# Performance work log

Measured on AMD Instinct MI355X. Metric: run time of the kernel, lower is better.

The kernel has to match this reference:

```python
import math
import jax, jax.numpy as jnp
from jax import lax
import numpy as np

NEG_INF = -1e9
LOG_2PI = math.log(2.0 * math.pi)


def compute_logp(z_p, m_p, logs_p):
    # z_p: [B,C,Ty], m_p/logs_p: [B,C,Tx] -> logp: [B,Tx,Ty]
    o_scale = jnp.exp(-2.0 * logs_p)                                  # [B,C,Tx]
    logp1 = jnp.sum(-0.5 * LOG_2PI - logs_p, axis=1)[:, :, None]      # [B,Tx,1]
    logp2 = jnp.einsum('bct,bcs->bts', o_scale, -0.5 * z_p ** 2)      # [B,Tx,Ty]
    logp3 = jnp.einsum('bct,bcs->bts', m_p * o_scale, z_p)            # [B,Tx,Ty]
    logp4 = jnp.sum(-0.5 * m_p ** 2 * o_scale, axis=1)[:, :, None]    # [B,Tx,1]
    return logp1 + logp2 + logp3 + logp4


def maximum_path(logp, mask):
    # Monotonic alignment search (Glow-TTS/VITS Viterbi DP).
    # logp, mask: [B,Tx,Ty]. Returns hard alignment path [B,Tx,Ty] in {0,1}.
    B, Tx, Ty = logp.shape
    tx = mask[:, :, 0].sum(axis=1).astype(jnp.int32)   # text lengths [B]
    ty = mask[:, 0, :].sum(axis=1).astype(jnp.int32)   # mel lengths  [B]
    xs = jnp.arange(Tx, dtype=jnp.int32)

    # ---- forward DP over mel frames y ----
    def fwd(v, inp):
        y, col = inp                                   # col: logp[:, :, y]  [B,Tx]
        v_stay = jnp.where(xs[None, :] == y, NEG_INF, v)           # can't stay on diagonal
        first = jnp.where(y == 0, 0.0, NEG_INF)                     # x==0 boundary
        v_move = jnp.concatenate([jnp.broadcast_to(first, (B, 1)).astype(v.dtype), v[:, :-1]], axis=1)
        newv = jnp.maximum(v_stay, v_move) + col
        # feasible band: x <= y and enough frames remain to consume all text
        feas = (xs[None, :] <= y) & (xs[None, :] >= tx[:, None] + y - ty[:, None])
        newv = jnp.where(feas, newv, NEG_INF)
        return newv, newv

    cols = jnp.moveaxis(logp, 2, 0)                    # [Ty,B,Tx]
    init = jnp.full((B, Tx), NEG_INF, dtype=logp.dtype)
    _, vals = lax.scan(fwd, init, (jnp.arange(Ty, dtype=jnp.int32), cols))  # [Ty,B,Tx]
    prev = jnp.concatenate([jnp.zeros((1, B, Tx), dtype=vals.dtype), vals[:-1]], axis=0)

    # ---- backtrack from (tx-1, ty-1) down to y=0 ----
    def bwd(idx, inp):
        y, pv = inp                                    # pv: value column at y-1  [B,Tx]
        active = y < ty                                # [B] bool
        path_col = (active[:, None] & (xs[None, :] == idx[:, None])).astype(logp.dtype)
        v_stay = jnp.take_along_axis(pv, idx[:, None], axis=1)[:, 0]
        v_move = jnp.take_along_axis(pv, jnp.maximum(idx - 1, 0)[:, None], axis=1)[:, 0]
        dec = (idx != 0) & ((idx == y) | (v_stay < v_move))
        idx = jnp.where(active & dec, idx - 1, idx)
        return idx, path_col

    _, path = lax.scan(bwd, tx - 1, (jnp.arange(Ty, dtype=jnp.int32), prev), reverse=True)
    return jnp.transpose(path, (1, 2, 0))              # [B,Tx,Ty]


def setup_inputs() -> dict:
    key = jax.random.key(0)
    ks = jax.random.split(key, 5)
    B, C, Tx, Ty = 16, 192, 384, 1536
    z_p = jax.random.normal(ks[0], (B, C, Ty), dtype=jnp.float32)
    m_p = jax.random.normal(ks[1], (B, C, Tx), dtype=jnp.float32)
    logs_p = 0.5 * jax.random.normal(ks[2], (B, C, Tx), dtype=jnp.float32)
    x_len = jax.random.randint(ks[3], (B,), Tx // 2, Tx + 1)
    y_len = jax.random.randint(ks[4], (B,), Ty // 2, Ty + 1)  # Ty//2 > Tx -> path always feasible
    x_mask = (jnp.arange(Tx)[None, :] < x_len[:, None]).astype(jnp.float32)[:, None, :]
    y_mask = (jnp.arange(Ty)[None, :] < y_len[:, None]).astype(jnp.float32)[:, None, :]
    return {"z_p": z_p, "m_p": m_p, "logs_p": logs_p, "x_mask": x_mask, "y_mask": y_mask}


def reference(z_p, m_p, logs_p, x_mask, y_mask):
    # forward_mas_without_dp: log-likelihood einsum + monotonic alignment search
    attn_mask = x_mask[:, 0, :, None] * y_mask[:, 0, None, :]   # [B,Tx,Ty]
    logp = compute_logp(z_p, m_p, logs_p)
    attn = maximum_path(logp, attn_mask)
    return attn[:, None]                                         # [B,1,Tx,Ty]
```

## Files before the change

### kernel.cpp

```cpp
#include <hip/hip_runtime.h>
#include <hip/hip_bf16.h>
#include <math.h>

#define NEG_INF (-1e9f)
#define B_   16
#define C_   192
#define TX   384
#define TY   1536
#define NWP  49
#define ROW_BYTES 1536

#define BM 64
#define BN 64
#define BK 16

typedef float f32x2 __attribute__((ext_vector_type(2)));
typedef float f32x4 __attribute__((ext_vector_type(4)));

__global__ __launch_bounds__(64) void k_len(const float* __restrict__ xm,
                                            const float* __restrict__ ym,
                                            int* __restrict__ lens) {
    const int b = blockIdx.x, l = threadIdx.x;
    int tx = 0, ty = 0;
#pragma unroll
    for (int i = 0; i < TX / 64; ++i)
        tx += __popcll(__ballot(xm[b * TX + i * 64 + l] > 0.5f));
#pragma unroll
    for (int i = 0; i < TY / 64; ++i)
        ty += __popcll(__ballot(ym[b * TY + i * 64 + l] > 0.5f));
    if (l == 0) { lens[2 * b] = tx; lens[2 * b + 1] = ty; }
}

__global__ __launch_bounds__(128) void k_rowconst(const float* __restrict__ m_p,
                                                  const float* __restrict__ logs_p,
                                                  float* __restrict__ r) {
    const int b = blockIdx.y;
    const int t = blockIdx.x * 128 + threadIdx.x;
    const float* mp = m_p + b * C_ * TX + t;
    const float* lp = logs_p + b * C_ * TX + t;
    const float c0 = -0.9189385332046727f;
    float s = 0.0f;
    for (int c = 0; c < C_; ++c) {
        float ls = lp[c * TX];
        float m  = mp[c * TX];
        float os = expf(-2.0f * ls);
        s += (c0 - ls) - 0.5f * m * m * os;
    }
    r[b * TX + t] = s;
}

__global__ __launch_bounds__(256) void k_logp(const float* __restrict__ z_p,
                                              const float* __restrict__ m_p,
                                              const float* __restrict__ logs_p,
                                              const float* __restrict__ r,
                                              const int* __restrict__ lens,
                                              float* __restrict__ outT) {
    const int L   = blockIdx.x;
    const int xcd = L & 7;
    const int j   = L >> 3;
    const int b   = xcd + 8 * (j & 1);
    const int jj  = j >> 1;
    const int sm0 = (23 - jj / 6) * BM;
    const int tn0 = (jj % 6) * BN;

    const int ty_len = lens[2 * b + 1];
    if (sm0 >= ((ty_len + 31) & ~31)) return;

    __shared__ float Zs1[BK][BM];
    __shared__ float Zs2[BK][BM];
    __shared__ float Ms1[BK][BN];
    __shared__ float Ms2[BK][BN];

    const int tid = threadIdx.x;
    const int lrow = tid >> 4;
    const int lcol = (tid & 15) << 2;
    const int tx_ = tid & 15;
    const int ty_ = tid >> 4;

    const float* mb = m_p + b * C_ * TX;
    const float* lb = logs_p + b * C_ * TX;
    const float* zb = z_p + b * C_ * TY;

    float acc[4][4] = {};

    for (int kk = 0; kk < C_; kk += BK) {
        float4 m4 = *(const float4*)(mb + (kk + lrow) * TX + tn0 + lcol);
        float4 l4 = *(const float4*)(lb + (kk + lrow) * TX + tn0 + lcol);
        float4 z4 = *(const float4*)(zb + (kk + lrow) * TY + sm0 + lcol);

        const float mm[4] = {m4.x, m4.y, m4.z, m4.w};
        const float ll[4] = {l4.x, l4.y, l4.z, l4.w};
        const float zz[4] = {z4.x, z4.y, z4.z, z4.w};
        float osv[4], a2v[4], u1v[4], u2v[4];
#pragma unroll
        for (int i = 0; i < 4; ++i) {
            float os = expf(-2.0f * ll[i]);
            osv[i] = os;
            a2v[i] = mm[i] * os;
            u1v[i] = -0.5f * zz[i] * zz[i];
            u2v[i] = zz[i];
        }

        __syncthreads();
#pragma unroll
        for (int i = 0; i < 4; ++i) {
            Ms1[lrow][lcol + i] = osv[i];
            Ms2[lrow][lcol + i] = a2v[i];
            Zs1[lrow][lcol + i] = u1v[i];
            Zs2[lrow][lcol + i] = u2v[i];
        }
        __syncthreads();

#pragma unroll
        for (int k = 0; k < BK; ++k) {
            float4 z1 = *(const float4*)&Zs1[k][ty_ * 4];
            float4 z2 = *(const float4*)&Zs2[k][ty_ * 4];
            float4 m1 = *(const float4*)&Ms1[k][tx_ * 4];
            float4 m2 = *(const float4*)&Ms2[k][tx_ * 4];
            const float u1a[4] = {z1.x, z1.y, z1.z, z1.w};
            const float u2a[4] = {z2.x, z2.y, z2.z, z2.w};
            const float a1a[4] = {m1.x, m1.y, m1.z, m1.w};
            const float a2a[4] = {m2.x, m2.y, m2.z, m2.w};
#pragma unroll
            for (int i = 0; i < 4; ++i)
#pragma unroll
                for (int j2 = 0; j2 < 4; ++j2)
                    acc[i][j2] = fmaf(a1a[j2], u1a[i], fmaf(a2a[j2], u2a[i], acc[i][j2]));
        }
    }

    float4 r4 = *(const float4*)(r + b * TX + tn0 + tx_ * 4);
    const float rr[4] = {r4.x, r4.y, r4.z, r4.w};
#pragma unroll
    for (int i = 0; i < 4; ++i) {
        const int srow = sm0 + ty_ * 4 + i;
        float4 o;
        o.x = acc[i][0] + rr[0];
        o.y = acc[i][1] + rr[1];
        o.z = acc[i][2] + rr[2];
        o.w = acc[i][3] + rr[3];
        *(float4*)(outT + ((size_t)(b * TY + srow)) * TX + tn0 + tx_ * 4) = o;
    }
}

__global__ __launch_bounds__(64) void k_dp(const float* __restrict__ logpT,
                                           const int* __restrict__ lens,
                                           int* __restrict__ idx_out) {
    extern __shared__ unsigned decw[];

    const int b = blockIdx.x;
    const int l = threadIdx.x;

    const int tx = lens[2 * b];
    const int ty = lens[2 * b + 1];
    const int yend = (ty + 31) & ~31;
    const int NBLK = yend >> 5;

    const char* pl = (const char*)(logpT + (size_t)b * TY * TX) + 24 * l;

    f32x4 Ra[16];
    f32x2 Rb[16];

#define ISSUE_ROW(u, row)                                                        \
    do {                                                                         \
        const char* _p = pl + (size_t)(row) * ROW_BYTES;                         \
        asm volatile("global_load_dwordx4 %0, %1, off"           : "=v"(Ra[u]) : "v"(_p)); \
        asm volatile("global_load_dwordx2 %0, %1, off offset:16" : "=v"(Rb[u]) : "v"(_p)); \
    } while (0)

#pragma unroll
    for (int u = 0; u < 16; ++u) ISSUE_ROW(u, u);

    float v[6];
    unsigned w[6];
#pragma unroll
    for (int k = 0; k < 6; ++k) { v[k] = NEG_INF; w[k] = 0u; }

    float lane0vm = 0.0f;
    const bool is_l0 = (l == 0);

    int nextrow = 16;
    for (int blk = 0; blk < NBLK; ++blk) {
#pragma unroll
        for (int j = 0; j < 32; ++j) {
            const int u = j & 15;
            asm volatile("s_waitcnt vmcnt(30)" : "+v"(Ra[u]), "+v"(Rb[u]));
            float c0 = Ra[u].x, c1 = Ra[u].y, c2 = Ra[u].z;
            float c3 = Ra[u].w, c4 = Rb[u].x, c5 = Rb[u].y;

            const int v5i = __float_as_int(v[5]);
            const int s15 = __builtin_amdgcn_readlane(v5i, 15);
            const int s31 = __builtin_amdgcn_readlane(v5i, 31);
            const int s47 = __builtin_amdgcn_readlane(v5i, 47);
            int vpi = __builtin_amdgcn_update_dpp(0, v5i, 0x111, 0xF, 0xF, false);
            asm("v_writelane_b32 %0, %1, 16" : "+v"(vpi) : "s"(s15));
            asm("v_writelane_b32 %0, %1, 32" : "+v"(vpi) : "s"(s31));
            asm("v_writelane_b32 %0, %1, 48" : "+v"(vpi) : "s"(s47));
            const float vp5 = __int_as_float(vpi);
            const float vm0 = is_l0 ? lane0vm : vp5;

            w[5] = w[5] + w[5] + (v[5] < v[4]);  float n5 = fmaxf(v[5], v[4]) + c5;
            w[4] = w[4] + w[4] + (v[4] < v[3]);  float n4 = fmaxf(v[4], v[3]) + c4;
            w[3] = w[3] + w[3] + (v[3] < v[2]);  float n3 = fmaxf(v[3], v[2]) + c3;
            w[2] = w[2] + w[2] + (v[2] < v[1]);  float n2 = fmaxf(v[2], v[1]) + c2;
            w[1] = w[1] + w[1] + (v[1] < v[0]);  float n1 = fmaxf(v[1], v[0]) + c1;
            w[0] = w[0] + w[0] + (v[0] < vm0);   float n0 = fmaxf(v[0], vm0) + c0;
            v[5] = n5; v[4] = n4; v[3] = n3; v[2] = n2; v[1] = n1; v[0] = n0;

            if (j == 0 && blk == 0) lane0vm = NEG_INF;

            {
                int nr = nextrow < TY ? nextrow : (TY - 1);
                ISSUE_ROW(u, nr);
                ++nextrow;
            }
        }
        const int x0 = 6 * l;
#pragma unroll
        for (int k = 0; k < 6; ++k) { decw[(x0 + k) * NWP + blk] = w[k]; w[k] = 0u; }
    }

    __syncthreads();

    for (int y = ty + l; y < TY; y += 64) idx_out[b * TY + y] = -1;

    if (l == 0) {
        int idx = tx - 1;
        int* io = idx_out + b * TY;
        int blk = (ty - 1) >> 5;
        auto W = [&](int i, int bb) -> unsigned {
            return (i >= 0) ? decw[i * NWP + bb] : 0u;
        };
        unsigned w0 = W(idx, blk), w1 = W(idx - 1, blk),
                 w2 = W(idx - 2, blk), w3 = W(idx - 3, blk);
        for (int y = ty - 1; y >= 0; --y) {
            const int nb = y >> 5;
            if (nb != blk) {
                blk = nb;
                w0 = W(idx, blk); w1 = W(idx - 1, blk);
                w2 = W(idx - 2, blk); w3 = W(idx - 3, blk);
            }
            io[y] = idx;
            if ((w0 >> (31 - (y & 31))) & 1u) {
                --idx;
                w0 = w1; w1 = w2; w2 = w3; w3 = W(idx - 3, blk);
            }
        }
    }
#undef ISSUE_ROW
}

__global__ __launch_bounds__(384) void k_path(const int* __restrict__ idx_arr,
                                              float* __restrict__ out) {
    const int b = blockIdx.y;
    const int x = blockIdx.x;
    const int t = threadIdx.x;
    const int y0 = t * 4;
    int4 iv = *(const int4*)(idx_arr + b * TY + y0);
    float4 o;
    o.x = (iv.x == x) ? 1.0f : 0.0f;
    o.y = (iv.y == x) ? 1.0f : 0.0f;
    o.z = (iv.z == x) ? 1.0f : 0.0f;
    o.w = (iv.w == x) ? 1.0f : 0.0f;
    *(float4*)(out + ((size_t)(b * TX + x)) * TY + y0) = o;
}

extern "C" void kernel_launch(void* const* d_in, const int* in_sizes, int n_in,
                              void* d_out, int out_size, void* d_ws, size_t ws_size,
                              hipStream_t stream) {
    const float* z_p    = (const float*)d_in[0];
    const float* m_p    = (const float*)d_in[1];
    const float* logs_p = (const float*)d_in[2];
    const float* x_mask = (const float*)d_in[3];
    const float* y_mask = (const float*)d_in[4];
    float* out = (float*)d_out;

    float* r       = (float*)d_ws;
    int*   idx_arr = (int*)((char*)d_ws + B_ * TX * 4);
    int*   lens    = (int*)((char*)d_ws + B_ * TX * 4 + B_ * TY * 4);

    static const size_t dp_smem = (size_t)TX * NWP * 4;
    (void)hipFuncSetAttribute((const void*)k_dp,
                              hipFuncAttributeMaxDynamicSharedMemorySize,
                              (int)dp_smem);

    k_len<<<B_, 64, 0, stream>>>(x_mask, y_mask, lens);
    k_rowconst<<<dim3(TX / 128, B_), 128, 0, stream>>>(m_p, logs_p, r);
    k_logp<<<24 * B_ * 6, 256, 0, stream>>>(z_p, m_p, logs_p, r, lens, out);
    k_dp<<<B_, 64, dp_smem, stream>>>(out, lens, idx_arr);
    k_path<<<dim3(TX, B_), TX, 0, stream>>>(idx_arr, out);
}
```

Measured before the change: 373.2 us.

## Add helper waves in DP kernel to prefetch logp rows into cache ahead of compute

The DP kernel grows from one wave to four. Wave 0 runs the serial Viterbi recurrence as before. The other three waves stride through the batch's logp buffer, issuing loads up to 128KB ahead of wave 0's published progress counter in shared memory, so its loads hit cache instead of HBM. The cost is extra load traffic, a spin-wait on a volatile shared counter, and possible contention with the critical wave.

```diff
diff --git a/kernel.cpp b/kernel.cpp
--- a/kernel.cpp
+++ b/kernel.cpp
@@ -9,6 +9,7 @@
 #define TY   1536
 #define NWP  49
 #define ROW_BYTES 1536
+#define DECW_BYTES (TX * NWP * 4)
 
 #define BM 64
 #define BN 64
@@ -143,24 +144,31 @@
     }
 }
 
-__global__ __launch_bounds__(64) void k_dp(const float* __restrict__ logpT,
-                                           const int* __restrict__ lens,
-                                           int* __restrict__ idx_out) {
-    extern __shared__ unsigned decw[];
-
-    const int b = blockIdx.x;
-    const int l = threadIdx.x;
+__global__ __launch_bounds__(256) void k_dp(const float* __restrict__ logpT,
+                                            const int* __restrict__ lens,
+                                            int* __restrict__ idx_out) {
+    extern __shared__ char smem[];
+    unsigned* decw = (unsigned*)smem;
+    volatile int* prog = (volatile int*)(smem + DECW_BYTES);
+
+    const int b   = blockIdx.x;
+    const int tid = threadIdx.x;
+    const int wid = tid >> 6;
+    const int l   = tid & 63;
 
     const int tx = lens[2 * b];
     const int ty = lens[2 * b + 1];
     const int yend = (ty + 31) & ~31;
     const int NBLK = yend >> 5;
 
-    const char* pl = (const char*)(logpT + (size_t)b * TY * TX) + 24 * l;
-
-    f32x4 Ra[16];
-    f32x2 Rb[16];
-
+    if (tid == 0) *prog = 0;
+    __syncthreads();
+
+    if (wid == 0) {
+        const char* pl = (const char*)(logpT + (size_t)b * TY * TX) + 24 * l;
+
+        f32x4 Ra[16];
+        f32x2 Rb[16];
 #define ISSUE_ROW(u, row)                                                        \
     do {                                                                         \
         const char* _p = pl + (size_t)(row) * ROW_BYTES;                         \
@@ -169,62 +177,75 @@
     } while (0)
 
 #pragma unroll
-    for (int u = 0; u < 16; ++u) ISSUE_ROW(u, u);
-
-    float v[6];
-    unsigned w[6];
-#pragma unroll
-    for (int k = 0; k < 6; ++k) { v[k] = NEG_INF; w[k] = 0u; }
-
-    float lane0vm = 0.0f;
-    const bool is_l0 = (l == 0);
-
-    int nextrow = 16;
-    for (int blk = 0; blk < NBLK; ++blk) {
-#pragma unroll
-        for (int j = 0; j < 32; ++j) {
-            const int u = j & 15;
-            asm volatile("s_waitcnt vmcnt(30)" : "+v"(Ra[u]), "+v"(Rb[u]));
-            float c0 = Ra[u].x, c1 = Ra[u].y, c2 = Ra[u].z;
-            float c3 = Ra[u].w, c4 = Rb[u].x, c5 = Rb[u].y;
-
-            const int v5i = __float_as_int(v[5]);
-            const int s15 = __builtin_amdgcn_readlane(v5i, 15);
-            const int s31 = __builtin_amdgcn_readlane(v5i, 31);
-            const int s47 = __builtin_amdgcn_readlane(v5i, 47);
-            int vpi = __builtin_amdgcn_update_dpp(0, v5i, 0x111, 0xF, 0xF, false);
-            asm("v_writelane_b32 %0, %1, 16" : "+v"(vpi) : "s"(s15));
-            asm("v_writelane_b32 %0, %1, 32" : "+v"(vpi) : "s"(s31));
-            asm("v_writelane_b32 %0, %1, 48" : "+v"(vpi) : "s"(s47));
-            const float vp5 = __int_as_float(vpi);
-            const float vm0 = is_l0 ? lane0vm : vp5;
-
-            w[5] = w[5] + w[5] + (v[5] < v[4]);  float n5 = fmaxf(v[5], v[4]) + c5;
-            w[4] = w[4] + w[4] + (v[4] < v[3]);  float n4 = fmaxf(v[4], v[3]) + c4;
-            w[3] = w[3] + w[3] + (v[3] < v[2]);  float n3 = fmaxf(v[3], v[2]) + c3;
-            w[2] = w[2] + w[2] + (v[2] < v[1]);  float n2 = fmaxf(v[2], v[1]) + c2;
-            w[1] = w[1] + w[1] + (v[1] < v[0]);  float n1 = fmaxf(v[1], v[0]) + c1;
-            w[0] = w[0] + w[0] + (v[0] < vm0);   float n0 = fmaxf(v[0], vm0) + c0;
-            v[5] = n5; v[4] = n4; v[3] = n3; v[2] = n2; v[1] = n1; v[0] = n0;
-
-            if (j == 0 && blk == 0) lane0vm = NEG_INF;
-
-            {
+        for (int u = 0; u < 16; ++u) ISSUE_ROW(u, u);
+
+        float v[6];
+        unsigned w[6];
+#pragma unroll
+        for (int k = 0; k < 6; ++k) { v[k] = NEG_INF; w[k] = 0u; }
+
+        float lane0vm = 0.0f;
+        const bool is_l0 = (l == 0);
+        int nextrow = 16;
+
+        for (int blk = 0; blk < NBLK; ++blk) {
+#pragma unroll
+            for (int j = 0; j < 32; ++j) {
+                const int u = j & 15;
+                asm volatile("s_waitcnt vmcnt(30)" : "+v"(Ra[u]), "+v"(Rb[u]));
+                float c0 = Ra[u].x, c1 = Ra[u].y, c2 = Ra[u].z;
+                float c3 = Ra[u].w, c4 = Rb[u].x, c5 = Rb[u].y;
+
+                const int v5i = __float_as_int(v[5]);
+                const int s15 = __builtin_amdgcn_readlane(v5i, 15);
+                const int s31 = __builtin_amdgcn_readlane(v5i, 31);
+                const int s47 = __builtin_amdgcn_readlane(v5i, 47);
+                int vpi = __builtin_amdgcn_update_dpp(0, v5i, 0x111, 0xF, 0xF, false);
+                asm("v_writelane_b32 %0, %1, 16" : "+v"(vpi) : "s"(s15));
+                asm("v_writelane_b32 %0, %1, 32" : "+v"(vpi) : "s"(s31));
+                asm("v_writelane_b32 %0, %1, 48" : "+v"(vpi) : "s"(s47));
+                const float vp5 = __int_as_float(vpi);
+                const float vm0 = is_l0 ? lane0vm : vp5;
+
+                w[5] = w[5] + w[5] + (v[5] < v[4]);  float n5 = fmaxf(v[5], v[4]) + c5;
+                w[4] = w[4] + w[4] + (v[4] < v[3]);  float n4 = fmaxf(v[4], v[3]) + c4;
+                w[3] = w[3] + w[3] + (v[3] < v[2]);  float n3 = fmaxf(v[3], v[2]) + c3;
+                w[2] = w[2] + w[2] + (v[2] < v[1]);  float n2 = fmaxf(v[2], v[1]) + c2;
+                w[1] = w[1] + w[1] + (v[1] < v[0]);  float n1 = fmaxf(v[1], v[0]) + c1;
+                w[0] = w[0] + w[0] + (v[0] < vm0);   float n0 = fmaxf(v[0], vm0) + c0;
+                v[5] = n5; v[4] = n4; v[3] = n3; v[2] = n2; v[1] = n1; v[0] = n0;
+
+                if (j == 0 && blk == 0) lane0vm = NEG_INF;
+
                 int nr = nextrow < TY ? nextrow : (TY - 1);
                 ISSUE_ROW(u, nr);
                 ++nextrow;
             }
-        }
-        const int x0 = 6 * l;
-#pragma unroll
-        for (int k = 0; k < 6; ++k) { decw[(x0 + k) * NWP + blk] = w[k]; w[k] = 0u; }
+            const int x0 = 6 * l;
+#pragma unroll
+            for (int k = 0; k < 6; ++k) { decw[(x0 + k) * NWP + blk] = w[k]; w[k] = 0u; }
+            if (l == 0) *prog = blk + 1;
+        }
+#undef ISSUE_ROW
+    } else {
+        const char* gb = (const char*)(logpT + (size_t)b * TY * TX);
+        const long total = (long)yend * ROW_BYTES;
+        float pd0, pd1;
+        for (long ci = (long)(wid - 1); ci * 8192 < total; ci += 3) {
+            while (ci * 8192 > (long)(*prog) * 32 * ROW_BYTES + 131072) { }
+            const char* p0 = gb + ci * 8192 + 64 * l;
+            const char* p1 = p0 + 4096;
+            asm volatile("global_load_dword %0, %1, off" : "=v"(pd0) : "v"(p0));
+            asm volatile("global_load_dword %0, %1, off" : "=v"(pd1) : "v"(p1));
+            asm volatile("s_waitcnt vmcnt(6)" ::: "memory");
+        }
     }
 
     __syncthreads();
 
-    for (int y = ty + l; y < TY; y += 64) idx_out[b * TY + y] = -1;
-
-    if (l == 0) {
+    for (int y = ty + tid; y < TY; y += 256) idx_out[b * TY + y] = -1;
+
+    if (tid == 0) {
         int idx = tx - 1;
         int* io = idx_out + b * TY;
         int blk = (ty - 1) >> 5;
@@ -247,7 +268,6 @@
             }
         }
     }
-#undef ISSUE_ROW
 }
 
 __global__ __launch_bounds__(384) void k_path(const int* __restrict__ idx_arr,
@@ -279,7 +299,7 @@
     int*   idx_arr = (int*)((char*)d_ws + B_ * TX * 4);
     int*   lens    = (int*)((char*)d_ws + B_ * TX * 4 + B_ * TY * 4);
 
-    static const size_t dp_smem = (size_t)TX * NWP * 4;
+    static const size_t dp_smem = DECW_BYTES + 16;
     (void)hipFuncSetAttribute((const void*)k_dp,
                               hipFuncAttributeMaxDynamicSharedMemorySize,
                               (int)dp_smem);
@@ -287,6 +307,6 @@
     k_len<<<B_, 64, 0, stream>>>(x_mask, y_mask, lens);
     k_rowconst<<<dim3(TX / 128, B_), 128, 0, stream>>>(m_p, logs_p, r);
     k_logp<<<24 * B_ * 6, 256, 0, stream>>>(z_p, m_p, logs_p, r, lens, out);
-    k_dp<<<B_, 64, dp_smem, stream>>>(out, lens, idx_arr);
+    k_dp<<<B_, 256, dp_smem, stream>>>(out, lens, idx_arr);
     k_path<<<dim3(TX, B_), TX, 0, stream>>>(idx_arr, out);
 }
```

After: 383.6 us. 2.8% more time.

## Add helper prefetch blocks that warm cache ahead of DP wavefronts

Applied to the files above, without the earlier changes.

The DP kernel launches three extra helper blocks per batch. Each one touches the upcoming logp rows a bounded distance ahead of the DP block's progress, so those rows are in cache when the serial DP reaches them. The DP block publishes its progress through a per-batch atomic counter, which k_len resets to zero. Helpers spin on that counter and each reserves the large dynamic shared memory allocation, so they can compete for CUs. The design also assumes the helpers are co-resident with the DP blocks they wait on.

```diff
diff --git a/kernel.cpp b/kernel.cpp
--- a/kernel.cpp
+++ b/kernel.cpp
@@ -9,6 +9,7 @@
 #define TY   1536
 #define NWP  49
 #define ROW_BYTES 1536
+#define DECW_BYTES (TX * NWP * 4)
 
 #define BM 64
 #define BN 64
@@ -19,8 +20,10 @@
 
 __global__ __launch_bounds__(64) void k_len(const float* __restrict__ xm,
                                             const float* __restrict__ ym,
-                                            int* __restrict__ lens) {
+                                            int* __restrict__ lens,
+                                            int* __restrict__ prog) {
     const int b = blockIdx.x, l = threadIdx.x;
+    if (l == 0) prog[b] = 0;
     int tx = 0, ty = 0;
 #pragma unroll
     for (int i = 0; i < TX / 64; ++i)
@@ -145,12 +148,36 @@
 
 __global__ __launch_bounds__(64) void k_dp(const float* __restrict__ logpT,
                                            const int* __restrict__ lens,
-                                           int* __restrict__ idx_out) {
+                                           int* __restrict__ idx_out,
+                                           int* __restrict__ prog) {
     extern __shared__ unsigned decw[];
 
-    const int b = blockIdx.x;
-    const int l = threadIdx.x;
-
+    const int bid = blockIdx.x;
+    const int l   = threadIdx.x;
+
+    if (bid >= B_) {
+        const int pb = bid - B_;
+        const int p  = pb >> 4;
+        const int bb = pb & 15;
+        const int ty2   = lens[2 * bb + 1];
+        const int yend2 = (ty2 + 31) & ~31;
+        const long total = (long)yend2 * ROW_BYTES;
+        const char* gb = (const char*)(logpT + (size_t)bb * TY * TX);
+        float d0, d1;
+        for (long ci = p; ci * 8192 < total; ci += 3) {
+            while ((long)__hip_atomic_load(&prog[bb], __ATOMIC_RELAXED,
+                                           __HIP_MEMORY_SCOPE_AGENT) * 49152
+                       + 262144 < ci * 8192) { }
+            const char* p0 = gb + ci * 8192 + 64 * (long)l;
+            asm volatile("global_load_dword %0, %1, off" : "=v"(d0) : "v"(p0));
+            asm volatile("global_load_dword %0, %1, off" : "=v"(d1) : "v"(p0 + 4096));
+            asm volatile("s_waitcnt vmcnt(6)" ::: "memory");
+        }
+        asm volatile("s_waitcnt vmcnt(0)" ::: "memory");
+        return;
+    }
+
+    const int b = bid;
     const int tx = lens[2 * b];
     const int ty = lens[2 * b + 1];
     const int yend = (ty + 31) & ~31;
@@ -218,6 +245,9 @@
         const int x0 = 6 * l;
 #pragma unroll
         for (int k = 0; k < 6; ++k) { decw[(x0 + k) * NWP + blk] = w[k]; w[k] = 0u; }
+        if (is_l0)
+            __hip_atomic_store(&prog[b], blk + 1, __ATOMIC_RELAXED,
+                               __HIP_MEMORY_SCOPE_AGENT);
     }
 
     __syncthreads();
@@ -228,8 +258,8 @@
         int idx = tx - 1;
         int* io = idx_out + b * TY;
         int blk = (ty - 1) >> 5;
-        auto W = [&](int i, int bb) -> unsigned {
-            return (i >= 0) ? decw[i * NWP + bb] : 0u;
+        auto W = [&](int i, int bb2) -> unsigned {
+            return (i >= 0) ? decw[i * NWP + bb2] : 0u;
         };
         unsigned w0 = W(idx, blk), w1 = W(idx - 1, blk),
                  w2 = W(idx - 2, blk), w3 = W(idx - 3, blk);
@@ -278,15 +308,16 @@
     float* r       = (float*)d_ws;
     int*   idx_arr = (int*)((char*)d_ws + B_ * TX * 4);
     int*   lens    = (int*)((char*)d_ws + B_ * TX * 4 + B_ * TY * 4);
+    int*   prog    = (int*)((char*)d_ws + B_ * TX * 4 + B_ * TY * 4 + 128);
 
     static const size_t dp_smem = (size_t)TX * NWP * 4;
     (void)hipFuncSetAttribute((const void*)k_dp,
                               hipFuncAttributeMaxDynamicSharedMemorySize,
                               (int)dp_smem);
 
-    k_len<<<B_, 64, 0, stream>>>(x_mask, y_mask, lens);
+    k_len<<<B_, 64, 0, stream>>>(x_mask, y_mask, lens, prog);
     k_rowconst<<<dim3(TX / 128, B_), 128, 0, stream>>>(m_p, logs_p, r);
     k_logp<<<24 * B_ * 6, 256, 0, stream>>>(z_p, m_p, logs_p, r, lens, out);
-    k_dp<<<B_, 64, dp_smem, stream>>>(out, lens, idx_arr);
+    k_dp<<<4 * B_, 64, dp_smem, stream>>>(out, lens, idx_arr, prog);
     k_path<<<dim3(TX, B_), TX, 0, stream>>>(idx_arr, out);
 }
```

Result: no change. 376.5 us (+0.9%).
